# Kernel optimization log

Measured on AMD Instinct MI355X. Metric: run time of the kernel, lower is better.

The kernel has to match this reference:

```python
import jax, jax.numpy as jnp
import numpy as np

GROUP_SIZE = 64
SCALING = 1.0  # lora_alpha / r = 16 / 16
# bitsandbytes NF4 codebook (16 normal-float levels)
NF4_CODE = jnp.array([
    -1.0, -0.6961928009986877, -0.5250730514526367, -0.39491748809814453,
    -0.28444138169288635, -0.18477343022823334, -0.09105003625154495, 0.0,
    0.07958029955625534, 0.16093020141124725, 0.24611230194568634,
    0.33791524171829224, 0.44070982933044434, 0.5626170039176941,
    0.7229568362236023, 1.0], dtype=jnp.float32)

IN_F, OUT_F, R, TOKENS = 4096, 11008, 16, 32


def setup_inputs() -> dict:
    key = jax.random.key(0)
    k0, k1, k2, k3, k4 = jax.random.split(key, 5)
    x = jax.random.normal(k0, (TOKENS, IN_F), dtype=jnp.float32)
    # each byte packs two 4-bit NF4 indices (high nibble first)
    packed_weight = jax.random.randint(k1, (OUT_F * IN_F // 2,), 0, 256, dtype=jnp.int32)
    # per-group absmax scales (positive)
    scales = jax.random.uniform(k2, (OUT_F * IN_F // GROUP_SIZE,), dtype=jnp.float32,
                                minval=0.005, maxval=0.05)
    lora_A = jax.random.normal(k3, (R, IN_F), dtype=jnp.float32) * 0.02
    lora_B = jax.random.normal(k4, (OUT_F, R), dtype=jnp.float32) * 0.02
    return {"x": x, "packed_weight": packed_weight, "scales": scales,
            "lora_A": lora_A, "lora_B": lora_B}


def _dequant_nf4(packed_weight, scales):
    hi = packed_weight // 16          # first nibble
    lo = packed_weight % 16           # second nibble
    idx = jnp.stack([hi, lo], axis=-1).reshape(-1)          # [out*in]
    w = NF4_CODE[idx].reshape(-1, GROUP_SIZE) * scales[:, None]
    return w.reshape(OUT_F, IN_F)                            # [out, in]


def reference(x, packed_weight, scales, lora_A, lora_B):
    W = _dequant_nf4(packed_weight, scales)
    base = x @ W.T                                           # [tokens, out]
    lora = (x @ lora_A.T) @ lora_B.T                         # low-rank update
    return base + SCALING * lora
```

## Files before the change

kernel.cpp:

```cpp
#include <hip/hip_runtime.h>
#include <hip/hip_bf16.h>

#define IN_F 4096
#define OUT_F 11008
#define TOKENS 32
#define RANK 16
#define KSPLIT 8
#define KSLICE (IN_F / KSPLIT)
#define XPAD 520
#define OUT_ELEMS (TOKENS * OUT_F)

typedef unsigned short u16;
typedef __attribute__((ext_vector_type(8))) short bf16x8;
typedef __attribute__((ext_vector_type(4))) float f32x4;
typedef __attribute__((ext_vector_type(4))) int i32x4;

__device__ const float NF4_d[16] = {
    -1.0f, -0.6961928009986877f, -0.5250730514526367f, -0.39491748809814453f,
    -0.28444138169288635f, -0.18477343022823334f, -0.09105003625154495f, 0.0f,
    0.07958029955625534f, 0.16093020141124725f, 0.24611230194568634f,
    0.33791524171829224f, 0.44070982933044434f, 0.5626170039176941f,
    0.7229568362236023f, 1.0f};

static __device__ __forceinline__ unsigned pk2(float a, float b) {
    __hip_bfloat162 h = __float22bfloat162_rn(make_float2(a, b));
    unsigned u;
    __builtin_memcpy(&u, &h, 4);
    return u;
}

__global__ void prep_xa_zero(const float* __restrict__ x, const float* __restrict__ A,
                             float* __restrict__ xa, float* __restrict__ out) {
    __shared__ float red[256];
    if (blockIdx.x >= 512) {
        int i = (blockIdx.x - 512) * 256 + threadIdx.x;
        float4 z = make_float4(0.f, 0.f, 0.f, 0.f);
        for (int j = i; j < OUT_ELEMS / 4; j += 16384) ((float4*)out)[j] = z;
        return;
    }
    int b = blockIdx.x;
    int t = b >> 4, r = b & 15;
    const float4* xr = (const float4*)(x + t * IN_F);
    const float4* ar = (const float4*)(A + r * IN_F);
    float s = 0.f;
    for (int c = 0; c < 4; ++c) {
        int j = c * 256 + threadIdx.x;
        float4 xv = xr[j], av = ar[j];
        s += xv.x * av.x + xv.y * av.y + xv.z * av.z + xv.w * av.w;
    }
    red[threadIdx.x] = s;
    __syncthreads();
    for (int st = 128; st > 0; st >>= 1) {
        if (threadIdx.x < st) red[threadIdx.x] += red[threadIdx.x + st];
        __syncthreads();
    }
    if (threadIdx.x == 0) xa[b] = red[0];
}

__global__ __launch_bounds__(256, 4) void qlora_fused(
    const int* __restrict__ packed, const float* __restrict__ scales,
    const float* __restrict__ x, const float* __restrict__ xa,
    const float* __restrict__ B, float* __restrict__ out) {
    __shared__ u16 xs[32 * XPAD];
    __shared__ unsigned tbl[256];
    __shared__ float xal[512];
    const int tid = threadIdx.x;
    const int kbase = blockIdx.y * KSLICE;
    const int obase = blockIdx.x * 64;

    const int lane = tid & 63;
    const int wv = tid >> 6;
    const int n = lane & 15;
    const int q = lane >> 4;
    const int o = obase + wv * 16 + n;

    const i32x4* ppq = (const i32x4*)(packed + o * 2048 + (kbase >> 1)) + q;
    i32x4 P[4];
    P[0] = __builtin_nontemporal_load(ppq);
    P[1] = __builtin_nontemporal_load(ppq + 4);
    P[2] = __builtin_nontemporal_load(ppq + 8);
    P[3] = __builtin_nontemporal_load(ppq + 12);

    const float4* sp = (const float4*)(scales + o * 64 + (kbase >> 6));
    float4 sA = sp[0], sB = sp[1];

    tbl[tid] = pk2(NF4_d[tid & 15], NF4_d[tid >> 4]);

    if (blockIdx.y == 0) {
        xal[tid] = xa[tid];
        xal[tid + 256] = xa[tid + 256];
    }

    for (int it = 0; it < 8; ++it) {
        int row = it * 4 + (tid >> 6);
        int c8 = tid & 63;
        const float4* src = (const float4*)(x + row * IN_F + kbase + c8 * 8);
        float4 v0 = src[0], v1 = src[1];
        uint4 d;
        d.x = pk2(v0.x, v0.y);
        d.y = pk2(v0.z, v0.w);
        d.z = pk2(v1.x, v1.y);
        d.w = pk2(v1.z, v1.w);
        *(uint4*)(xs + row * XPAD + c8 * 8) = d;
    }
    __syncthreads();

    f32x4 acc0 = {0.f, 0.f, 0.f, 0.f};
    f32x4 acc1 = {0.f, 0.f, 0.f, 0.f};
    const u16* xr0 = xs + n * XPAD + q * 8;
    const u16* xr1 = xs + (n + 16) * XPAD + q * 8;
    const float scr[8] = {sA.x, sA.y, sA.z, sA.w, sB.x, sB.y, sB.z, sB.w};

#pragma unroll
    for (int s = 0; s < 16; ++s) {
        i32x4 cur = P[s & 3];
        if (s + 4 < 16) P[s & 3] = __builtin_nontemporal_load(ppq + (s + 4) * 4);
        float sc = scr[s >> 1];

        unsigned u0 = tbl[cur[0] & 255];
        unsigned u1 = tbl[cur[1] & 255];
        unsigned u2 = tbl[cur[2] & 255];
        unsigned u3 = tbl[cur[3] & 255];
        uint4 bu;
        bu.x = pk2(__int_as_float(u0 & 0xFFFF0000u) * sc, __int_as_float(u0 << 16) * sc);
        bu.y = pk2(__int_as_float(u1 & 0xFFFF0000u) * sc, __int_as_float(u1 << 16) * sc);
        bu.z = pk2(__int_as_float(u2 & 0xFFFF0000u) * sc, __int_as_float(u2 << 16) * sc);
        bu.w = pk2(__int_as_float(u3 & 0xFFFF0000u) * sc, __int_as_float(u3 << 16) * sc);
        bf16x8 bfrag;
        __builtin_memcpy(&bfrag, &bu, 16);
        bf16x8 a0 = *(const bf16x8*)(xr0 + s * 32);
        bf16x8 a1 = *(const bf16x8*)(xr1 + s * 32);
        acc0 = __builtin_amdgcn_mfma_f32_16x16x32_bf16(a0, bfrag, acc0, 0, 0, 0);
        acc1 = __builtin_amdgcn_mfma_f32_16x16x32_bf16(a1, bfrag, acc1, 0, 0, 0);
    }

    float lora[8] = {0.f, 0.f, 0.f, 0.f, 0.f, 0.f, 0.f, 0.f};
    if (blockIdx.y == 0) {
        const float4* br = (const float4*)(B + o * RANK);
        float4 b0 = br[0], b1 = br[1], b2 = br[2], b3 = br[3];
#pragma unroll
        for (int r = 0; r < 4; ++r) {
            const float* x0 = xal + (q * 4 + r) * RANK;
            const float* x1 = xal + (q * 4 + r + 16) * RANK;
            float s0 = 0.f, s1 = 0.f;
#pragma unroll
            for (int j = 0; j < 4; ++j) {
                const float4 bj = ((const float4*)&b0)[0];
            }
            s0 = b0.x * x0[0] + b0.y * x0[1] + b0.z * x0[2] + b0.w * x0[3] +
                 b1.x * x0[4] + b1.y * x0[5] + b1.z * x0[6] + b1.w * x0[7] +
                 b2.x * x0[8] + b2.y * x0[9] + b2.z * x0[10] + b2.w * x0[11] +
                 b3.x * x0[12] + b3.y * x0[13] + b3.z * x0[14] + b3.w * x0[15];
            s1 = b0.x * x1[0] + b0.y * x1[1] + b0.z * x1[2] + b0.w * x1[3] +
                 b1.x * x1[4] + b1.y * x1[5] + b1.z * x1[6] + b1.w * x1[7] +
                 b2.x * x1[8] + b2.y * x1[9] + b2.z * x1[10] + b2.w * x1[11] +
                 b3.x * x1[12] + b3.y * x1[13] + b3.z * x1[14] + b3.w * x1[15];
            lora[r] = s0;
            lora[r + 4] = s1;
        }
    }

#pragma unroll
    for (int r = 0; r < 4; ++r) {
        int t = q * 4 + r;
        atomicAdd(out + t * OUT_F + o, acc0[r] + lora[r]);
        atomicAdd(out + (t + 16) * OUT_F + o, acc1[r] + lora[r + 4]);
    }
}

extern "C" void kernel_launch(void* const* d_in, const int* in_sizes, int n_in,
                              void* d_out, int out_size, void* d_ws, size_t ws_size,
                              hipStream_t stream) {
    const float* x = (const float*)d_in[0];
    const int* packed = (const int*)d_in[1];
    const float* scales = (const float*)d_in[2];
    const float* lora_A = (const float*)d_in[3];
    const float* lora_B = (const float*)d_in[4];
    float* out = (float*)d_out;

    float* xa = (float*)d_ws;

    prep_xa_zero<<<576, 256, 0, stream>>>(x, lora_A, xa, out);
    qlora_fused<<<dim3(OUT_F / 64, KSPLIT), 256, 0, stream>>>(packed, scales, x, xa,
                                                              lora_B, out);
}
```

Before: 152.7 us.

## Switch to 32x32x16 MFMA with post-MFMA group scaling and finer K split

Replaces the pair of 16x16x32 MFMAs per step with 32x32x16 MFMAs, so one wave covers all 32 tokens against 32 output columns. The per-group scale is no longer applied to each dequantized weight; raw NF4 bf16 codes from the table go straight into the MFMA, and each 64-element group's partial sum is scaled in fp32 afterwards. This removes the per-element multiply and bf16 repack from the dequant path. KSPLIT doubles to 16 to keep enough blocks with 128 outputs per block, which doubles the number of atomic adds into the output. The LoRA reduction in the prep kernel now uses wave shuffles instead of a shared-memory tree.

```diff
diff --git a/kernel.cpp b/kernel.cpp
--- a/kernel.cpp
+++ b/kernel.cpp
@@ -5,14 +5,14 @@
 #define OUT_F 11008
 #define TOKENS 32
 #define RANK 16
-#define KSPLIT 8
+#define KSPLIT 16
 #define KSLICE (IN_F / KSPLIT)
-#define XPAD 520
+#define XP 264
 #define OUT_ELEMS (TOKENS * OUT_F)
 
 typedef unsigned short u16;
 typedef __attribute__((ext_vector_type(8))) short bf16x8;
-typedef __attribute__((ext_vector_type(4))) float f32x4;
+typedef __attribute__((ext_vector_type(16))) float f32x16;
 typedef __attribute__((ext_vector_type(4))) int i32x4;
 
 __device__ const float NF4_d[16] = {
@@ -31,7 +31,6 @@
 
 __global__ void prep_xa_zero(const float* __restrict__ x, const float* __restrict__ A,
                              float* __restrict__ xa, float* __restrict__ out) {
-    __shared__ float red[256];
     if (blockIdx.x >= 512) {
         int i = (blockIdx.x - 512) * 256 + threadIdx.x;
         float4 z = make_float4(0.f, 0.f, 0.f, 0.f);
@@ -48,123 +47,121 @@
         float4 xv = xr[j], av = ar[j];
         s += xv.x * av.x + xv.y * av.y + xv.z * av.z + xv.w * av.w;
     }
-    red[threadIdx.x] = s;
+    for (int off = 32; off > 0; off >>= 1) s += __shfl_down(s, off, 64);
+    __shared__ float w4[4];
+    if ((threadIdx.x & 63) == 0) w4[threadIdx.x >> 6] = s;
     __syncthreads();
-    for (int st = 128; st > 0; st >>= 1) {
-        if (threadIdx.x < st) red[threadIdx.x] += red[threadIdx.x + st];
-        __syncthreads();
-    }
-    if (threadIdx.x == 0) xa[b] = red[0];
+    if (threadIdx.x == 0) xa[b] = w4[0] + w4[1] + w4[2] + w4[3];
 }
 
 __global__ __launch_bounds__(256, 4) void qlora_fused(
     const int* __restrict__ packed, const float* __restrict__ scales,
     const float* __restrict__ x, const float* __restrict__ xa,
     const float* __restrict__ B, float* __restrict__ out) {
-    __shared__ u16 xs[32 * XPAD];
+    __shared__ u16 xs[32 * XP];
     __shared__ unsigned tbl[256];
     __shared__ float xal[512];
     const int tid = threadIdx.x;
-    const int kbase = blockIdx.y * KSLICE;
-    const int obase = blockIdx.x * 64;
-
     const int lane = tid & 63;
     const int wv = tid >> 6;
-    const int n = lane & 15;
-    const int q = lane >> 4;
-    const int o = obase + wv * 16 + n;
+    const int n = lane & 31;
+    const int h = lane >> 5;
+    const int kbase = blockIdx.y * KSLICE;
+    const int o = blockIdx.x * 128 + wv * 32 + n;
 
-    const i32x4* ppq = (const i32x4*)(packed + o * 2048 + (kbase >> 1)) + q;
-    i32x4 P[4];
-    P[0] = __builtin_nontemporal_load(ppq);
-    P[1] = __builtin_nontemporal_load(ppq + 4);
-    P[2] = __builtin_nontemporal_load(ppq + 8);
-    P[3] = __builtin_nontemporal_load(ppq + 12);
+    const i32x4* ppq = (const i32x4*)(packed + o * 2048 + (kbase >> 1) + h * 4);
+    i32x4 Pa[2], Pb[2];
+    Pa[0] = __builtin_nontemporal_load(ppq + 0);
+    Pb[0] = __builtin_nontemporal_load(ppq + 2);
+    Pa[1] = __builtin_nontemporal_load(ppq + 4);
+    Pb[1] = __builtin_nontemporal_load(ppq + 6);
 
-    const float4* sp = (const float4*)(scales + o * 64 + (kbase >> 6));
-    float4 sA = sp[0], sB = sp[1];
+    float4 sv = *(const float4*)(scales + o * 64 + (kbase >> 6));
+    const float scr[4] = {sv.x, sv.y, sv.z, sv.w};
 
-    tbl[tid] = pk2(NF4_d[tid & 15], NF4_d[tid >> 4]);
+    tbl[tid] = pk2(NF4_d[tid >> 4], NF4_d[tid & 15]);
 
     if (blockIdx.y == 0) {
         xal[tid] = xa[tid];
         xal[tid + 256] = xa[tid + 256];
     }
 
-    for (int it = 0; it < 8; ++it) {
-        int row = it * 4 + (tid >> 6);
-        int c8 = tid & 63;
-        const float4* src = (const float4*)(x + row * IN_F + kbase + c8 * 8);
-        float4 v0 = src[0], v1 = src[1];
-        uint4 d;
-        d.x = pk2(v0.x, v0.y);
-        d.y = pk2(v0.z, v0.w);
-        d.z = pk2(v1.x, v1.y);
-        d.w = pk2(v1.z, v1.w);
-        *(uint4*)(xs + row * XPAD + c8 * 8) = d;
+    {
+        int row = tid >> 3;
+        int c = (tid & 7) * 32;
+        const float4* src = (const float4*)(x + row * IN_F + kbase + c);
+        u16* dst = xs + row * XP + c;
+#pragma unroll
+        for (int j = 0; j < 4; ++j) {
+            float4 a = src[j * 2], b2 = src[j * 2 + 1];
+            uint4 d;
+            d.x = pk2(a.x, a.y);
+            d.y = pk2(a.z, a.w);
+            d.z = pk2(b2.x, b2.y);
+            d.w = pk2(b2.z, b2.w);
+            *(uint4*)(dst + j * 8) = d;
+        }
     }
     __syncthreads();
 
-    f32x4 acc0 = {0.f, 0.f, 0.f, 0.f};
-    f32x4 acc1 = {0.f, 0.f, 0.f, 0.f};
-    const u16* xr0 = xs + n * XPAD + q * 8;
-    const u16* xr1 = xs + (n + 16) * XPAD + q * 8;
-    const float scr[8] = {sA.x, sA.y, sA.z, sA.w, sB.x, sB.y, sB.z, sB.w};
+    f32x16 acc = {};
+    f32x16 sub;
+    const f32x16 Z = {};
+    const u16* ar = xs + (lane & 31) * XP + h * 8;
 
 #pragma unroll
-    for (int s = 0; s < 16; ++s) {
-        i32x4 cur = P[s & 3];
-        if (s + 4 < 16) P[s & 3] = __builtin_nontemporal_load(ppq + (s + 4) * 4);
-        float sc = scr[s >> 1];
-
-        unsigned u0 = tbl[cur[0] & 255];
-        unsigned u1 = tbl[cur[1] & 255];
-        unsigned u2 = tbl[cur[2] & 255];
-        unsigned u3 = tbl[cur[3] & 255];
-        uint4 bu;
-        bu.x = pk2(__int_as_float(u0 & 0xFFFF0000u) * sc, __int_as_float(u0 << 16) * sc);
-        bu.y = pk2(__int_as_float(u1 & 0xFFFF0000u) * sc, __int_as_float(u1 << 16) * sc);
-        bu.z = pk2(__int_as_float(u2 & 0xFFFF0000u) * sc, __int_as_float(u2 << 16) * sc);
-        bu.w = pk2(__int_as_float(u3 & 0xFFFF0000u) * sc, __int_as_float(u3 << 16) * sc);
-        bf16x8 bfrag;
-        __builtin_memcpy(&bfrag, &bu, 16);
-        bf16x8 a0 = *(const bf16x8*)(xr0 + s * 32);
-        bf16x8 a1 = *(const bf16x8*)(xr1 + s * 32);
-        acc0 = __builtin_amdgcn_mfma_f32_16x16x32_bf16(a0, bfrag, acc0, 0, 0, 0);
-        acc1 = __builtin_amdgcn_mfma_f32_16x16x32_bf16(a1, bfrag, acc1, 0, 0, 0);
+    for (int s = 0; s < 8; ++s) {
+        i32x4 ca = Pa[s & 1], cb = Pb[s & 1];
+        if (s + 2 < 8) {
+            Pa[s & 1] = __builtin_nontemporal_load(ppq + (s + 2) * 4);
+            Pb[s & 1] = __builtin_nontemporal_load(ppq + (s + 2) * 4 + 2);
+        }
+        uint4 b0u, b1u;
+        b0u.x = tbl[ca[0] & 255];
+        b0u.y = tbl[ca[1] & 255];
+        b0u.z = tbl[ca[2] & 255];
+        b0u.w = tbl[ca[3] & 255];
+        b1u.x = tbl[cb[0] & 255];
+        b1u.y = tbl[cb[1] & 255];
+        b1u.z = tbl[cb[2] & 255];
+        b1u.w = tbl[cb[3] & 255];
+        bf16x8 bf0, bf1;
+        __builtin_memcpy(&bf0, &b0u, 16);
+        __builtin_memcpy(&bf1, &b1u, 16);
+        bf16x8 a0 = *(const bf16x8*)(ar + s * 32);
+        bf16x8 a1 = *(const bf16x8*)(ar + s * 32 + 16);
+        if ((s & 1) == 0) {
+            sub = __builtin_amdgcn_mfma_f32_32x32x16_bf16(a0, bf0, Z, 0, 0, 0);
+            sub = __builtin_amdgcn_mfma_f32_32x32x16_bf16(a1, bf1, sub, 0, 0, 0);
+        } else {
+            sub = __builtin_amdgcn_mfma_f32_32x32x16_bf16(a0, bf0, sub, 0, 0, 0);
+            sub = __builtin_amdgcn_mfma_f32_32x32x16_bf16(a1, bf1, sub, 0, 0, 0);
+            float sc = scr[s >> 1];
+#pragma unroll
+            for (int i = 0; i < 16; ++i) acc[i] += sc * sub[i];
+        }
     }
 
-    float lora[8] = {0.f, 0.f, 0.f, 0.f, 0.f, 0.f, 0.f, 0.f};
     if (blockIdx.y == 0) {
         const float4* br = (const float4*)(B + o * RANK);
         float4 b0 = br[0], b1 = br[1], b2 = br[2], b3 = br[3];
 #pragma unroll
-        for (int r = 0; r < 4; ++r) {
-            const float* x0 = xal + (q * 4 + r) * RANK;
-            const float* x1 = xal + (q * 4 + r + 16) * RANK;
-            float s0 = 0.f, s1 = 0.f;
+        for (int i = 0; i < 16; ++i) {
+            int t = (i & 3) + 8 * (i >> 2) + 4 * h;
+            const float4* xt = (const float4*)(xal + t * RANK);
+            float4 x0 = xt[0], x1 = xt[1], x2 = xt[2], x3 = xt[3];
+            float lor = b0.x * x0.x + b0.y * x0.y + b0.z * x0.z + b0.w * x0.w +
+                        b1.x * x1.x + b1.y * x1.y + b1.z * x1.z + b1.w * x1.w +
+                        b2.x * x2.x + b2.y * x2.y + b2.z * x2.z + b2.w * x2.w +
+                        b3.x * x3.x + b3.y * x3.y + b3.z * x3.z + b3.w * x3.w;
+            atomicAdd(out + t * OUT_F + o, acc[i] + lor);
+        }
+    } else {
 #pragma unroll
-            for (int j = 0; j < 4; ++j) {
-                const float4 bj = ((const float4*)&b0)[0];
-            }
-            s0 = b0.x * x0[0] + b0.y * x0[1] + b0.z * x0[2] + b0.w * x0[3] +
-                 b1.x * x0[4] + b1.y * x0[5] + b1.z * x0[6] + b1.w * x0[7] +
-                 b2.x * x0[8] + b2.y * x0[9] + b2.z * x0[10] + b2.w * x0[11] +
-                 b3.x * x0[12] + b3.y * x0[13] + b3.z * x0[14] + b3.w * x0[15];
-            s1 = b0.x * x1[0] + b0.y * x1[1] + b0.z * x1[2] + b0.w * x1[3] +
-                 b1.x * x1[4] + b1.y * x1[5] + b1.z * x1[6] + b1.w * x1[7] +
-                 b2.x * x1[8] + b2.y * x1[9] + b2.z * x1[10] + b2.w * x1[11] +
-                 b3.x * x1[12] + b3.y * x1[13] + b3.z * x1[14] + b3.w * x1[15];
-            lora[r] = s0;
-            lora[r + 4] = s1;
+        for (int i = 0; i < 16; ++i) {
+            int t = (i & 3) + 8 * (i >> 2) + 4 * h;
+            atomicAdd(out + t * OUT_F + o, acc[i]);
         }
-    }
-
-#pragma unroll
-    for (int r = 0; r < 4; ++r) {
-        int t = q * 4 + r;
-        atomicAdd(out + t * OUT_F + o, acc0[r] + lora[r]);
-        atomicAdd(out + (t + 16) * OUT_F + o, acc1[r] + lora[r + 4]);
     }
 }
 
@@ -181,6 +178,6 @@
     float* xa = (float*)d_ws;
 
     prep_xa_zero<<<576, 256, 0, stream>>>(x, lora_A, xa, out);
-    qlora_fused<<<dim3(OUT_F / 64, KSPLIT), 256, 0, stream>>>(packed, scales, x, xa,
-                                                              lora_B, out);
+    qlora_fused<<<dim3(OUT_F / 128, KSPLIT), 256, 0, stream>>>(packed, scales, x, xa,
+                                                               lora_B, out);
 }
```

After: 165.7 us. +8.5%, slower.

## Process two 16-column output tiles per wave to reuse x fragments

Applied to the files above, without the earlier changes.

Each wave now computes 32 output columns (two 16-wide tiles) instead of 16, so each block covers 128 outputs and the grid halves along the output dimension. The bf16 x tile staged in shared memory is converted and loaded once per block and reused across twice as many weight columns, and each A fragment feeds two MFMAs. The weight prefetch depth drops from 4 to 2 stages per stream to limit register growth, which risks more exposed memory latency and lower occupancy. Halving the block count also means the per-block x conversion prologue runs half as often.

```diff
diff --git a/kernel.cpp b/kernel.cpp
--- a/kernel.cpp
+++ b/kernel.cpp
@@ -66,23 +66,26 @@
     __shared__ float xal[512];
     const int tid = threadIdx.x;
     const int kbase = blockIdx.y * KSLICE;
-    const int obase = blockIdx.x * 64;
 
     const int lane = tid & 63;
     const int wv = tid >> 6;
     const int n = lane & 15;
     const int q = lane >> 4;
-    const int o = obase + wv * 16 + n;
-
-    const i32x4* ppq = (const i32x4*)(packed + o * 2048 + (kbase >> 1)) + q;
-    i32x4 P[4];
-    P[0] = __builtin_nontemporal_load(ppq);
-    P[1] = __builtin_nontemporal_load(ppq + 4);
-    P[2] = __builtin_nontemporal_load(ppq + 8);
-    P[3] = __builtin_nontemporal_load(ppq + 12);
-
-    const float4* sp = (const float4*)(scales + o * 64 + (kbase >> 6));
-    float4 sA = sp[0], sB = sp[1];
+    const int olo = blockIdx.x * 128 + wv * 32 + n;
+    const int ohi = olo + 16;
+
+    const i32x4* pp0 = (const i32x4*)(packed + olo * 2048 + (kbase >> 1)) + q;
+    const i32x4* pp1 = (const i32x4*)(packed + ohi * 2048 + (kbase >> 1)) + q;
+    i32x4 P0[2], P1[2];
+    P0[0] = __builtin_nontemporal_load(pp0);
+    P1[0] = __builtin_nontemporal_load(pp1);
+    P0[1] = __builtin_nontemporal_load(pp0 + 4);
+    P1[1] = __builtin_nontemporal_load(pp1 + 4);
+
+    const float4* sp0 = (const float4*)(scales + olo * 64 + (kbase >> 6));
+    const float4* sp1 = (const float4*)(scales + ohi * 64 + (kbase >> 6));
+    float4 s0A = sp0[0], s0B = sp0[1];
+    float4 s1A = sp1[0], s1B = sp1[1];
 
     tbl[tid] = pk2(NF4_d[tid & 15], NF4_d[tid >> 4]);
 
@@ -105,66 +108,90 @@
     }
     __syncthreads();
 
-    f32x4 acc0 = {0.f, 0.f, 0.f, 0.f};
-    f32x4 acc1 = {0.f, 0.f, 0.f, 0.f};
+    f32x4 acc00 = {0.f, 0.f, 0.f, 0.f};
+    f32x4 acc10 = {0.f, 0.f, 0.f, 0.f};
+    f32x4 acc01 = {0.f, 0.f, 0.f, 0.f};
+    f32x4 acc11 = {0.f, 0.f, 0.f, 0.f};
     const u16* xr0 = xs + n * XPAD + q * 8;
     const u16* xr1 = xs + (n + 16) * XPAD + q * 8;
-    const float scr[8] = {sA.x, sA.y, sA.z, sA.w, sB.x, sB.y, sB.z, sB.w};
+    const float sc0r[8] = {s0A.x, s0A.y, s0A.z, s0A.w, s0B.x, s0B.y, s0B.z, s0B.w};
+    const float sc1r[8] = {s1A.x, s1A.y, s1A.z, s1A.w, s1B.x, s1B.y, s1B.z, s1B.w};
 
 #pragma unroll
     for (int s = 0; s < 16; ++s) {
-        i32x4 cur = P[s & 3];
-        if (s + 4 < 16) P[s & 3] = __builtin_nontemporal_load(ppq + (s + 4) * 4);
-        float sc = scr[s >> 1];
-
-        unsigned u0 = tbl[cur[0] & 255];
-        unsigned u1 = tbl[cur[1] & 255];
-        unsigned u2 = tbl[cur[2] & 255];
-        unsigned u3 = tbl[cur[3] & 255];
-        uint4 bu;
-        bu.x = pk2(__int_as_float(u0 & 0xFFFF0000u) * sc, __int_as_float(u0 << 16) * sc);
-        bu.y = pk2(__int_as_float(u1 & 0xFFFF0000u) * sc, __int_as_float(u1 << 16) * sc);
-        bu.z = pk2(__int_as_float(u2 & 0xFFFF0000u) * sc, __int_as_float(u2 << 16) * sc);
-        bu.w = pk2(__int_as_float(u3 & 0xFFFF0000u) * sc, __int_as_float(u3 << 16) * sc);
-        bf16x8 bfrag;
-        __builtin_memcpy(&bfrag, &bu, 16);
+        i32x4 c0 = P0[s & 1];
+        i32x4 c1 = P1[s & 1];
+        if (s + 2 < 16) {
+            P0[s & 1] = __builtin_nontemporal_load(pp0 + (s + 2) * 4);
+            P1[s & 1] = __builtin_nontemporal_load(pp1 + (s + 2) * 4);
+        }
+        float sc0 = sc0r[s >> 1];
+        float sc1 = sc1r[s >> 1];
+
+        uint4 b0u, b1u;
+        {
+            unsigned u0 = tbl[c0[0] & 255], u1 = tbl[c0[1] & 255];
+            unsigned u2 = tbl[c0[2] & 255], u3 = tbl[c0[3] & 255];
+            b0u.x = pk2(__int_as_float(u0 & 0xFFFF0000u) * sc0, __int_as_float(u0 << 16) * sc0);
+            b0u.y = pk2(__int_as_float(u1 & 0xFFFF0000u) * sc0, __int_as_float(u1 << 16) * sc0);
+            b0u.z = pk2(__int_as_float(u2 & 0xFFFF0000u) * sc0, __int_as_float(u2 << 16) * sc0);
+            b0u.w = pk2(__int_as_float(u3 & 0xFFFF0000u) * sc0, __int_as_float(u3 << 16) * sc0);
+        }
+        {
+            unsigned u0 = tbl[c1[0] & 255], u1 = tbl[c1[1] & 255];
+            unsigned u2 = tbl[c1[2] & 255], u3 = tbl[c1[3] & 255];
+            b1u.x = pk2(__int_as_float(u0 & 0xFFFF0000u) * sc1, __int_as_float(u0 << 16) * sc1);
+            b1u.y = pk2(__int_as_float(u1 & 0xFFFF0000u) * sc1, __int_as_float(u1 << 16) * sc1);
+            b1u.z = pk2(__int_as_float(u2 & 0xFFFF0000u) * sc1, __int_as_float(u2 << 16) * sc1);
+            b1u.w = pk2(__int_as_float(u3 & 0xFFFF0000u) * sc1, __int_as_float(u3 << 16) * sc1);
+        }
+        bf16x8 bf0, bf1;
+        __builtin_memcpy(&bf0, &b0u, 16);
+        __builtin_memcpy(&bf1, &b1u, 16);
         bf16x8 a0 = *(const bf16x8*)(xr0 + s * 32);
         bf16x8 a1 = *(const bf16x8*)(xr1 + s * 32);
-        acc0 = __builtin_amdgcn_mfma_f32_16x16x32_bf16(a0, bfrag, acc0, 0, 0, 0);
-        acc1 = __builtin_amdgcn_mfma_f32_16x16x32_bf16(a1, bfrag, acc1, 0, 0, 0);
-    }
-
-    float lora[8] = {0.f, 0.f, 0.f, 0.f, 0.f, 0.f, 0.f, 0.f};
+        acc00 = __builtin_amdgcn_mfma_f32_16x16x32_bf16(a0, bf0, acc00, 0, 0, 0);
+        acc10 = __builtin_amdgcn_mfma_f32_16x16x32_bf16(a1, bf0, acc10, 0, 0, 0);
+        acc01 = __builtin_amdgcn_mfma_f32_16x16x32_bf16(a0, bf1, acc01, 0, 0, 0);
+        acc11 = __builtin_amdgcn_mfma_f32_16x16x32_bf16(a1, bf1, acc11, 0, 0, 0);
+    }
+
     if (blockIdx.y == 0) {
-        const float4* br = (const float4*)(B + o * RANK);
-        float4 b0 = br[0], b1 = br[1], b2 = br[2], b3 = br[3];
+        const float4* brl = (const float4*)(B + olo * RANK);
+        const float4* brh = (const float4*)(B + ohi * RANK);
+        float4 l0 = brl[0], l1 = brl[1], l2 = brl[2], l3 = brl[3];
+        float4 h0 = brh[0], h1 = brh[1], h2 = brh[2], h3 = brh[3];
 #pragma unroll
         for (int r = 0; r < 4; ++r) {
-            const float* x0 = xal + (q * 4 + r) * RANK;
-            const float* x1 = xal + (q * 4 + r + 16) * RANK;
-            float s0 = 0.f, s1 = 0.f;
-#pragma unroll
-            for (int j = 0; j < 4; ++j) {
-                const float4 bj = ((const float4*)&b0)[0];
+            int t = q * 4 + r;
+#pragma unroll
+            for (int half = 0; half < 2; ++half) {
+                int tt = t + half * 16;
+                const float4* xt = (const float4*)(xal + tt * RANK);
+                float4 x0 = xt[0], x1 = xt[1], x2 = xt[2], x3 = xt[3];
+                float lorL = l0.x * x0.x + l0.y * x0.y + l0.z * x0.z + l0.w * x0.w +
+                             l1.x * x1.x + l1.y * x1.y + l1.z * x1.z + l1.w * x1.w +
+                             l2.x * x2.x + l2.y * x2.y + l2.z * x2.z + l2.w * x2.w +
+                             l3.x * x3.x + l3.y * x3.y + l3.z * x3.z + l3.w * x3.w;
+                float lorH = h0.x * x0.x + h0.y * x0.y + h0.z * x0.z + h0.w * x0.w +
+                             h1.x * x1.x + h1.y * x1.y + h1.z * x1.z + h1.w * x1.w +
+                             h2.x * x2.x + h2.y * x2.y + h2.z * x2.z + h2.w * x2.w +
+                             h3.x * x3.x + h3.y * x3.y + h3.z * x3.z + h3.w * x3.w;
+                float aL = half ? acc10[r] : acc00[r];
+                float aH = half ? acc11[r] : acc01[r];
+                atomicAdd(out + tt * OUT_F + olo, aL + lorL);
+                atomicAdd(out + tt * OUT_F + ohi, aH + lorH);
             }
-            s0 = b0.x * x0[0] + b0.y * x0[1] + b0.z * x0[2] + b0.w * x0[3] +
-                 b1.x * x0[4] + b1.y * x0[5] + b1.z * x0[6] + b1.w * x0[7] +
-                 b2.x * x0[8] + b2.y * x0[9] + b2.z * x0[10] + b2.w * x0[11] +
-                 b3.x * x0[12] + b3.y * x0[13] + b3.z * x0[14] + b3.w * x0[15];
-            s1 = b0.x * x1[0] + b0.y * x1[1] + b0.z * x1[2] + b0.w * x1[3] +
-                 b1.x * x1[4] + b1.y * x1[5] + b1.z * x1[6] + b1.w * x1[7] +
-                 b2.x * x1[8] + b2.y * x1[9] + b2.z * x1[10] + b2.w * x1[11] +
-                 b3.x * x1[12] + b3.y * x1[13] + b3.z * x1[14] + b3.w * x1[15];
-            lora[r] = s0;
-            lora[r + 4] = s1;
-        }
-    }
-
-#pragma unroll
-    for (int r = 0; r < 4; ++r) {
-        int t = q * 4 + r;
-        atomicAdd(out + t * OUT_F + o, acc0[r] + lora[r]);
-        atomicAdd(out + (t + 16) * OUT_F + o, acc1[r] + lora[r + 4]);
+        }
+    } else {
+#pragma unroll
+        for (int r = 0; r < 4; ++r) {
+            int t = q * 4 + r;
+            atomicAdd(out + t * OUT_F + olo, acc00[r]);
+            atomicAdd(out + (t + 16) * OUT_F + olo, acc10[r]);
+            atomicAdd(out + t * OUT_F + ohi, acc01[r]);
+            atomicAdd(out + (t + 16) * OUT_F + ohi, acc11[r]);
+        }
     }
 }
 
@@ -181,6 +208,6 @@
     float* xa = (float*)d_ws;
 
     prep_xa_zero<<<576, 256, 0, stream>>>(x, lora_A, xa, out);
-    qlora_fused<<<dim3(OUT_F / 64, KSPLIT), 256, 0, stream>>>(packed, scales, x, xa,
-                                                              lora_B, out);
-}
+    qlora_fused<<<dim3(OUT_F / 128, KSPLIT), 256, 0, stream>>>(packed, scales, x, xa,
+                                                               lora_B, out);
+}
```

After: 152.8 us. About the same (+0.1%).
